# Kernel tuning notes

Hardware: AMD Instinct MI355X
Metric: run time of the kernel (lower is better)

## Reference

```python
import jax, jax.numpy as jnp
import numpy as np

N = 30000
E = 480000
C_IN, H = 16, 4
NEG_SLOPE = 0.2  # PyG GATv2Conv default negative_slope


def gatv2(x, src, dst, Wl, bl, Wr, br, att, bias, heads, outc, concat, n):
    # PyG GATv2Conv (share_weights=False): e_ij = att . leaky_relu(Wl x_j + Wr x_i)
    xl = (x @ Wl + bl).reshape(n, heads, outc)   # source transform
    xr = (x @ Wr + br).reshape(n, heads, outc)   # target transform
    e = jax.nn.leaky_relu(xl[src] + xr[dst], NEG_SLOPE)        # [E,H,C]
    logits = jnp.einsum('ehc,hc->eh', e, att)                  # [E,H]
    m = jax.lax.stop_gradient(jax.ops.segment_max(logits, dst, num_segments=n))
    ex = jnp.exp(logits - m[dst])
    denom = jax.ops.segment_sum(ex, dst, num_segments=n)
    alpha = ex / denom[dst]                                    # scatter-softmax over in-edges
    out = jax.ops.segment_sum(alpha[:, :, None] * xl[src], dst, num_segments=n)  # [N,H,C]
    out = out.reshape(n, heads * outc) if concat else out.mean(axis=1)
    return out + bias


def setup_inputs() -> dict:
    key = jax.random.key(0)
    ks = jax.random.split(key, 16)
    s = 0.05
    inp = {
        'x': jax.random.uniform(ks[0], (N, C_IN), dtype=jnp.float32),
        'edge_index': jax.random.randint(ks[1], (2, E), 0, N, dtype=jnp.int32),
        'lower_bound': jnp.zeros((C_IN,), jnp.float32),
        'upper_bound': jnp.ones((C_IN,), jnp.float32),
        # Layer 1: GATv2Conv(16 -> 32 per head, heads=4, concat=True) => 128
        'W1l': jax.random.normal(ks[2], (C_IN, H * 32), jnp.float32) * s,
        'b1l': jnp.zeros((H * 32,), jnp.float32),
        'W1r': jax.random.normal(ks[3], (C_IN, H * 32), jnp.float32) * s,
        'b1r': jnp.zeros((H * 32,), jnp.float32),
        'att1': jax.random.normal(ks[4], (H, 32), jnp.float32) * s,
        'bias1': jnp.zeros((H * 32,), jnp.float32),
        # Layer 2: GATv2Conv(128 -> 64 per head, heads=4, concat=False) => 64
        'W2l': jax.random.normal(ks[5], (128, H * 64), jnp.float32) * s,
        'b2l': jnp.zeros((H * 64,), jnp.float32),
        'W2r': jax.random.normal(ks[6], (128, H * 64), jnp.float32) * s,
        'b2r': jnp.zeros((H * 64,), jnp.float32),
        'att2': jax.random.normal(ks[7], (H, 64), jnp.float32) * s,
        'bias2': jnp.zeros((64,), jnp.float32),
        # Final linear head 64 -> 5
        'W3': jax.random.normal(ks[8], (64, 5), jnp.float32) * s,
        'b3': jnp.zeros((5,), jnp.float32),
    }
    return inp


def reference(x, edge_index, lower_bound, upper_bound,
              W1l, b1l, W1r, b1r, att1, bias1,
              W2l, b2l, W2r, b2r, att2, bias2,
              W3, b3):
    n = x.shape[0]
    # min-max normalization
    y = (x - lower_bound) / (upper_bound - lower_bound)
    # add self loops (PyG GATv2Conv default add_self_loops=True)
    loops = jnp.tile(jnp.arange(n, dtype=edge_index.dtype)[None, :], (2, 1))
    ei = jnp.concatenate([edge_index, loops], axis=1)
    src, dst = ei[0], ei[1]
    y = gatv2(y, src, dst, W1l, b1l, W1r, b1r, att1, bias1, H, 32, True, n)
    y = jax.nn.relu(y)
    y = gatv2(y, src, dst, W2l, b2l, W2r, b2r, att2, bias2, H, 64, False, n)
    y = jax.nn.relu(y)
    y = y @ W3 + b3
    return jax.nn.sigmoid(y)
```

## Files before the change

kernel.cpp:

```cpp
#include <hip/hip_runtime.h>

#define H 4
#define D1 128
#define D2 256
#define CIN 16
#define SLOPE 0.2f
#define LOG2E 1.4426950408889634f

typedef short short8v __attribute__((ext_vector_type(8)));
typedef float float4v __attribute__((ext_vector_type(4)));
typedef __fp16 half2v __attribute__((ext_vector_type(2)));

__device__ __forceinline__ unsigned short f2bf(float f) {
    unsigned int u = __float_as_uint(f);
    u += 0x7FFFu + ((u >> 16) & 1u);
    return (unsigned short)(u >> 16);
}
__device__ __forceinline__ half2v pkrtz(float a, float b) {
    return __builtin_amdgcn_cvt_pkrtz(a, b);
}
__device__ __forceinline__ half2v h2_from_u32(unsigned u) {
    return __builtin_bit_cast(half2v, u);
}
__device__ __forceinline__ unsigned u32_from_h2(half2v h) {
    return __builtin_bit_cast(unsigned, h);
}
__device__ __forceinline__ float fdot2(half2v a, half2v b, float c) {
#if __has_builtin(__builtin_amdgcn_fdot2)
    return __builtin_amdgcn_fdot2(a, b, c, false);
#else
    return c + (float)a.x * (float)b.x + (float)a.y * (float)b.y;
#endif
}

__device__ __forceinline__ float dpp_sum16(float x) {
    float t;
    t = __int_as_float(__builtin_amdgcn_mov_dpp(__float_as_int(x), 0xB1, 0xF, 0xF, true));
    x += t;
    t = __int_as_float(__builtin_amdgcn_mov_dpp(__float_as_int(x), 0x4E, 0xF, 0xF, true));
    x += t;
    t = __int_as_float(__builtin_amdgcn_mov_dpp(__float_as_int(x), 0x141, 0xF, 0xF, true));
    x += t;
    t = __int_as_float(__builtin_amdgcn_mov_dpp(__float_as_int(x), 0x140, 0xF, 0xF, true));
    x += t;
    return x;
}

__global__ void k_hist(const int* __restrict__ ei, int E, int ET,
                       int* __restrict__ deg) {
    int idx = blockIdx.x * blockDim.x + threadIdx.x;
    if (idx >= ET) return;
    int dst = (idx < E) ? ei[E + idx] : idx - E;
    atomicAdd(&deg[dst], 1);
}

__global__ __launch_bounds__(1024) void k_scan_one(
        const int* __restrict__ deg, int* __restrict__ rp,
        int* __restrict__ cur, int n) {
    __shared__ int wsum[16];
    int t = threadIdx.x;
    int lane = t & 63, w = t >> 6;
    int base = t * 32;
    int vals[32];
    const int4* dp = (const int4*)deg;
#pragma unroll
    for (int q = 0; q < 8; ++q) {
        int4 v = dp[(base >> 2) + q];
        vals[4 * q + 0] = v.x; vals[4 * q + 1] = v.y;
        vals[4 * q + 2] = v.z; vals[4 * q + 3] = v.w;
    }
    int loc[32];
    int s = 0;
#pragma unroll
    for (int k = 0; k < 32; ++k) {
        int idx = base + k;
        int v = (idx < n) ? vals[k] : 0;
        loc[k] = s;
        s += v;
    }
    int inc = s;
#pragma unroll
    for (int off = 1; off < 64; off <<= 1) {
        int u = __shfl_up(inc, off, 64);
        if (lane >= off) inc += u;
    }
    int excl = inc - s;
    if (lane == 63) wsum[w] = inc;
    __syncthreads();
    if (w == 0) {
        int v = (lane < 16) ? wsum[lane] : 0;
        int winc = v;
#pragma unroll
        for (int off = 1; off < 16; off <<= 1) {
            int u = __shfl_up(winc, off, 64);
            if (lane >= off) winc += u;
        }
        if (lane < 16) wsum[lane] = winc - v;
    }
    __syncthreads();
    int offw = wsum[w] + excl;
#pragma unroll
    for (int q = 0; q < 8; ++q) {
        int i0 = base + 4 * q;
        if (i0 + 3 < n) {
            *(int4*)(rp + i0) = make_int4(offw + loc[4 * q + 0], offw + loc[4 * q + 1],
                                          offw + loc[4 * q + 2], offw + loc[4 * q + 3]);
            *(int4*)(cur + i0) = make_int4(0, 0, 0, 0);
        } else {
#pragma unroll
            for (int e = 0; e < 4; ++e) {
                int idx = i0 + e;
                if (idx < n) { rp[idx] = offw + loc[4 * q + e]; cur[idx] = 0; }
            }
        }
    }
}

__global__ void k_fill(const int* __restrict__ ei, int E, int ET,
                       const int* __restrict__ rp, int* __restrict__ cur,
                       int* __restrict__ eord) {
    int idx = blockIdx.x * blockDim.x + threadIdx.x;
    if (idx >= ET) return;
    int src, dst;
    if (idx < E) { src = ei[idx]; dst = ei[E + idx]; }
    else         { src = dst = idx - E; }
    int pos = atomicAdd(&cur[dst], 1);
    eord[rp[dst] + pos] = src;
}

__global__ __launch_bounds__(256) void k_prep(
        const float* __restrict__ x, const float* __restrict__ lb,
        const float* __restrict__ ub,
        const float* __restrict__ Wl, const float* __restrict__ bl,
        const float* __restrict__ Wr, const float* __restrict__ br,
        unsigned short* __restrict__ xl16, unsigned short* __restrict__ xr16,
        const float* __restrict__ W2l, const float* __restrict__ W2r,
        unsigned short* __restrict__ W2t,
        int* __restrict__ deg, int n, int B1) {
    __shared__ float Wls[CIN][D1];
    __shared__ float Wrs[CIN][D1];
    __shared__ float ys[16][CIN];
    int b = blockIdx.x;
    int t = threadIdx.x;
    if (b >= B1) {
        int rb = b - B1;
        if (rb < 256) {
            int idx = rb * 256 + t;
            int k = idx >> 9, c = idx & 511;
            float v = (c < 256) ? W2l[k * 256 + c] : W2r[k * 256 + (c - 256)];
            W2t[(size_t)c * 128 + k] = f2bf(v);
        } else {
            int idx = (rb - 256) * 256 + t;
            if (idx < n) deg[idx] = 0;
        }
        return;
    }
    int i0 = b * 16;
#pragma unroll
    for (int i = 0; i < 8; ++i) {
        int flat = t + 256 * i;
        int k = flat >> 7, c = flat & 127;
        Wls[k][c] = Wl[k * D1 + c];
        Wrs[k][c] = Wr[k * D1 + c];
    }
    {
        int node = t >> 4, k = t & 15;
        int gi = i0 + node;
        float xv = (gi < n) ? x[(size_t)gi * CIN + k] : 0.f;
        ys[node][k] = (xv - lb[k]) / (ub[k] - lb[k]);
    }
    __syncthreads();
    int c = t & 127;
    bool left = t < 128;
    const float (*Ws)[D1] = left ? Wls : Wrs;
    float bias = left ? bl[c] : br[c];
    unsigned short* obuf = left ? xl16 : xr16;
    for (int j = 0; j < 16; ++j) {
        float acc = bias;
#pragma unroll
        for (int k = 0; k < CIN; ++k) acc += ys[j][k] * Ws[k][c];
        int gi = i0 + j;
        float other = __shfl_xor(acc, 1);
        if (gi < n && !(c & 1))
            *(unsigned*)(obuf + (size_t)gi * D1 + c) = u32_from_h2(pkrtz(acc, other));
    }
}

__global__ __launch_bounds__(256) void k_lin2_mfma(
        const unsigned short* __restrict__ h1b,
        const unsigned short* __restrict__ W2t,
        const float* __restrict__ b2l, const float* __restrict__ b2r,
        unsigned short* __restrict__ xl2,
        unsigned short* __restrict__ xr2,
        int n) {
    __shared__ unsigned short At[128 * 128];
    __shared__ unsigned short Bt[128 * 128];
    int t = threadIdx.x;
    int row0 = blockIdx.x * 128;
    int col0 = blockIdx.y * 128;

    {
        int r = t >> 1, hh = (t & 1) * 64;
        bool ok = (row0 + r) < n;
        const unsigned short* gA = h1b + (size_t)(row0 + r) * 128 + hh;
        const unsigned short* gB = W2t + (size_t)(col0 + r) * 128 + hh;
#pragma unroll
        for (int i = 0; i < 8; ++i) {
            uint4 vA = ok ? *(const uint4*)(gA + i * 8) : make_uint4(0, 0, 0, 0);
            uint4 vB = *(const uint4*)(gB + i * 8);
            int col = hh + i * 8;
            int idx = (r * 128 + col) ^ ((r & 15) << 3);
            *(uint4*)&At[idx] = vA;
            *(uint4*)&Bt[idx] = vB;
        }
    }
    __syncthreads();

    int w = t >> 6, l = t & 63;
    int wr = w >> 1, wc = w & 1;
    float4v acc[4][4];
#pragma unroll
    for (int m = 0; m < 4; ++m)
#pragma unroll
        for (int nn = 0; nn < 4; ++nn) acc[m][nn] = (float4v)0.f;

#pragma unroll
    for (int ks = 0; ks < 4; ++ks) {
        int kb = ks * 32 + ((l >> 4) << 3);
        short8v a[4], b[4];
#pragma unroll
        for (int m = 0; m < 4; ++m) {
            int r = wr * 64 + m * 16 + (l & 15);
            a[m] = *(const short8v*)&At[(r * 128 + kb) ^ ((r & 15) << 3)];
        }
#pragma unroll
        for (int nn = 0; nn < 4; ++nn) {
            int c = wc * 64 + nn * 16 + (l & 15);
            b[nn] = *(const short8v*)&Bt[(c * 128 + kb) ^ ((c & 15) << 3)];
        }
#pragma unroll
        for (int m = 0; m < 4; ++m)
#pragma unroll
            for (int nn = 0; nn < 4; ++nn)
                acc[m][nn] = __builtin_amdgcn_mfma_f32_16x16x32_bf16(
                    a[m], b[nn], acc[m][nn], 0, 0, 0);
    }

    unsigned short* ob = (col0 < 256) ? xl2 : xr2;
    const float* bp = (col0 < 256) ? b2l : b2r;
    int cb = (col0 < 256) ? col0 : col0 - 256;
#pragma unroll
    for (int nn = 0; nn < 4; ++nn) {
        int colc = cb + wc * 64 + nn * 16 + (l & 15);
        float bv = bp[colc];
#pragma unroll
        for (int m = 0; m < 4; ++m) {
            int rbase = row0 + wr * 64 + m * 16 + ((l >> 4) << 2);
#pragma unroll
            for (int r = 0; r < 4; ++r) {
                int row = rbase + r;
                float val = acc[m][nn][r] + bv;
                float other = __shfl_xor(val, 1);
                if (!(l & 1) && row < n)
                    *(unsigned*)(ob + (size_t)row * 256 + colc) =
                        u32_from_h2(pkrtz(val, other));
            }
        }
    }
}

__global__ __launch_bounds__(256) void k_agg1(
        const unsigned short* __restrict__ xl16, const unsigned short* __restrict__ xr16,
        const float* __restrict__ att, const float* __restrict__ bias,
        const int* __restrict__ rp, const int* __restrict__ deg,
        const int* __restrict__ eord, unsigned short* __restrict__ h1b, int n) {
    int t = threadIdx.x;
    int node = blockIdx.x * 4 + (t >> 6);
    int l = t & 63;
    int nd = (node < n) ? node : n - 1;
    half2v xr01 = h2_from_u32(((const unsigned*)xr16)[(size_t)nd * 64 + l]);
    float2 av = *(const float2*)(att + 2 * l);
    half2v av01 = pkrtz(av.x * LOG2E, av.y * LOG2E);
    half2v slp = pkrtz(SLOPE, SLOPE);
    int start = __builtin_amdgcn_readfirstlane(rp[nd]);
    int cnt   = (node < n) ? deg[nd] : 0;
    cnt = __builtin_amdgcn_readfirstlane(cnt);
    const unsigned* xlp = (const unsigned*)xl16;
    float d = 0.f;
    half2v a01 = pkrtz(0.f, 0.f);
    int cnt4 = cnt & ~3;
    unsigned r0, r1, r2, r3;
    if (cnt4 > 0) {
        int i0 = eord[start + 0], i1 = eord[start + 1];
        int i2 = eord[start + 2], i3 = eord[start + 3];
        r0 = xlp[(size_t)i0 * 64 + l]; r1 = xlp[(size_t)i1 * 64 + l];
        r2 = xlp[(size_t)i2 * 64 + l]; r3 = xlp[(size_t)i3 * 64 + l];
    }
    for (int j = 0; j < cnt4; j += 4) {
        half2v x0 = h2_from_u32(r0), x1 = h2_from_u32(r1);
        half2v x2 = h2_from_u32(r2), x3 = h2_from_u32(r3);
        int jn = j + 4;
        if (jn < cnt4) {
            int i0 = eord[start + jn + 0], i1 = eord[start + jn + 1];
            int i2 = eord[start + jn + 2], i3 = eord[start + jn + 3];
            r0 = xlp[(size_t)i0 * 64 + l]; r1 = xlp[(size_t)i1 * 64 + l];
            r2 = xlp[(size_t)i2 * 64 + l]; r3 = xlp[(size_t)i3 * 64 + l];
        }
        half2v s0 = x0 + xr01, s1 = x1 + xr01, s2 = x2 + xr01, s3 = x3 + xr01;
        s0 = __builtin_elementwise_max(s0, s0 * slp);
        s1 = __builtin_elementwise_max(s1, s1 * slp);
        s2 = __builtin_elementwise_max(s2, s2 * slp);
        s3 = __builtin_elementwise_max(s3, s3 * slp);
        float lg0 = fdot2(av01, s0, 0.f);
        float lg1 = fdot2(av01, s1, 0.f);
        float lg2 = fdot2(av01, s2, 0.f);
        float lg3 = fdot2(av01, s3, 0.f);
        lg0 = dpp_sum16(lg0); lg1 = dpp_sum16(lg1);
        lg2 = dpp_sum16(lg2); lg3 = dpp_sum16(lg3);
        float e0 = exp2f(lg0), e1 = exp2f(lg1);
        float e2 = exp2f(lg2), e3 = exp2f(lg3);
        d += (e0 + e1) + (e2 + e3);
        a01 += pkrtz(e0, e0) * x0;
        a01 += pkrtz(e1, e1) * x1;
        a01 += pkrtz(e2, e2) * x2;
        a01 += pkrtz(e3, e3) * x3;
    }
    for (int j = cnt4; j < cnt; ++j) {
        int s0i = eord[start + j];
        half2v x0 = h2_from_u32(xlp[(size_t)s0i * 64 + l]);
        half2v s0 = x0 + xr01;
        s0 = __builtin_elementwise_max(s0, s0 * slp);
        float lg0 = fdot2(av01, s0, 0.f);
        lg0 = dpp_sum16(lg0);
        float e0 = exp2f(lg0);
        d += e0;
        a01 += pkrtz(e0, e0) * x0;
    }
    if (node < n) {
        float inv = 1.f / d;
        float o0 = fmaxf((float)a01.x * inv + bias[2 * l + 0], 0.f);
        float o1 = fmaxf((float)a01.y * inv + bias[2 * l + 1], 0.f);
        ((unsigned*)h1b)[(size_t)node * 64 + l] =
            ((unsigned)f2bf(o1) << 16) | f2bf(o0);
    }
}

__global__ __launch_bounds__(256) void k_agg2(
        const unsigned short* __restrict__ xl16, const unsigned short* __restrict__ xr16,
        const float* __restrict__ att, const float* __restrict__ b2,
        const float* __restrict__ W3, const float* __restrict__ b3,
        const int* __restrict__ rp, const int* __restrict__ deg,
        const int* __restrict__ eord, float* __restrict__ out, int n) {
    int t = threadIdx.x;
    int node = blockIdx.x * 4 + (t >> 6);
    int l = t & 63;
    int nd = (node < n) ? node : n - 1;
    uint2 xru = ((const uint2*)xr16)[(size_t)nd * 64 + l];
    half2v xr01 = h2_from_u32(xru.x), xr23 = h2_from_u32(xru.y);
    float4 av = *(const float4*)(att + 4 * l);
    half2v av01 = pkrtz(av.x * LOG2E, av.y * LOG2E);
    half2v av23 = pkrtz(av.z * LOG2E, av.w * LOG2E);
    half2v slp = pkrtz(SLOPE, SLOPE);
    int start = __builtin_amdgcn_readfirstlane(rp[nd]);
    int cnt   = (node < n) ? deg[nd] : 0;
    cnt = __builtin_amdgcn_readfirstlane(cnt);
    const uint2* xlp = (const uint2*)xl16;
    float d = 0.f;
    half2v a01 = pkrtz(0.f, 0.f), a23 = pkrtz(0.f, 0.f);
    int cnt4 = cnt & ~3;
    uint2 r0, r1, r2, r3;
    if (cnt4 > 0) {
        int i0 = eord[start + 0], i1 = eord[start + 1];
        int i2 = eord[start + 2], i3 = eord[start + 3];
        r0 = xlp[(size_t)i0 * 64 + l]; r1 = xlp[(size_t)i1 * 64 + l];
        r2 = xlp[(size_t)i2 * 64 + l]; r3 = xlp[(size_t)i3 * 64 + l];
    }
    for (int j = 0; j < cnt4; j += 4) {
        half2v x00 = h2_from_u32(r0.x), x01p = h2_from_u32(r0.y);
        half2v x10 = h2_from_u32(r1.x), x11p = h2_from_u32(r1.y);
        half2v x20 = h2_from_u32(r2.x), x21p = h2_from_u32(r2.y);
        half2v x30 = h2_from_u32(r3.x), x31p = h2_from_u32(r3.y);
        int jn = j + 4;
        if (jn < cnt4) {
            int i0 = eord[start + jn + 0], i1 = eord[start + jn + 1];
            int i2 = eord[start + jn + 2], i3 = eord[start + jn + 3];
            r0 = xlp[(size_t)i0 * 64 + l]; r1 = xlp[(size_t)i1 * 64 + l];
            r2 = xlp[(size_t)i2 * 64 + l]; r3 = xlp[(size_t)i3 * 64 + l];
        }
        half2v s;
        float lg0, lg1, lg2, lg3;
        s = x00 + xr01; s = __builtin_elementwise_max(s, s * slp);
        lg0 = fdot2(av01, s, 0.f);
        s = x01p + xr23; s = __builtin_elementwise_max(s, s * slp);
        lg0 = fdot2(av23, s, lg0);
        s = x10 + xr01; s = __builtin_elementwise_max(s, s * slp);
        lg1 = fdot2(av01, s, 0.f);
        s = x11p + xr23; s = __builtin_elementwise_max(s, s * slp);
        lg1 = fdot2(av23, s, lg1);
        s = x20 + xr01; s = __builtin_elementwise_max(s, s * slp);
        lg2 = fdot2(av01, s, 0.f);
        s = x21p + xr23; s = __builtin_elementwise_max(s, s * slp);
        lg2 = fdot2(av23, s, lg2);
        s = x30 + xr01; s = __builtin_elementwise_max(s, s * slp);
        lg3 = fdot2(av01, s, 0.f);
        s = x31p + xr23; s = __builtin_elementwise_max(s, s * slp);
        lg3 = fdot2(av23, s, lg3);
        lg0 = dpp_sum16(lg0); lg1 = dpp_sum16(lg1);
        lg2 = dpp_sum16(lg2); lg3 = dpp_sum16(lg3);
        float e0 = exp2f(lg0), e1 = exp2f(lg1);
        float e2 = exp2f(lg2), e3 = exp2f(lg3);
        d += (e0 + e1) + (e2 + e3);
        half2v ep;
        ep = pkrtz(e0, e0); a01 += ep * x00; a23 += ep * x01p;
        ep = pkrtz(e1, e1); a01 += ep * x10; a23 += ep * x11p;
        ep = pkrtz(e2, e2); a01 += ep * x20; a23 += ep * x21p;
        ep = pkrtz(e3, e3); a01 += ep * x30; a23 += ep * x31p;
    }
    for (int j = cnt4; j < cnt; ++j) {
        int s0i = eord[start + j];
        uint2 p0 = xlp[(size_t)s0i * 64 + l];
        half2v x00 = h2_from_u32(p0.x), x01p = h2_from_u32(p0.y);
        half2v s;
        float lg0;
        s = x00 + xr01; s = __builtin_elementwise_max(s, s * slp);
        lg0 = fdot2(av01, s, 0.f);
        s = x01p + xr23; s = __builtin_elementwise_max(s, s * slp);
        lg0 = fdot2(av23, s, lg0);
        lg0 = dpp_sum16(lg0);
        float e0 = exp2f(lg0);
        d += e0;
        half2v ep = pkrtz(e0, e0);
        a01 += ep * x00; a23 += ep * x01p;
    }
    float inv = 1.f / d;
    float v0 = (float)a01.x * inv, v1 = (float)a01.y * inv;
    float v2 = (float)a23.x * inv, v3 = (float)a23.y * inv;
    v0 += __shfl_xor(v0, 16); v1 += __shfl_xor(v1, 16);
    v2 += __shfl_xor(v2, 16); v3 += __shfl_xor(v3, 16);
    v0 += __shfl_xor(v0, 32); v1 += __shfl_xor(v1, 32);
    v2 += __shfl_xor(v2, 32); v3 += __shfl_xor(v3, 32);
    int c0 = 4 * (l & 15);
    v0 = fmaxf(0.25f * v0 + b2[c0 + 0], 0.f);
    v1 = fmaxf(0.25f * v1 + b2[c0 + 1], 0.f);
    v2 = fmaxf(0.25f * v2 + b2[c0 + 2], 0.f);
    v3 = fmaxf(0.25f * v3 + b2[c0 + 3], 0.f);
    float p0, p1, p2, p3, p4;
    {
        const float* w0 = W3 + (c0 + 0) * 5;
        const float* w1 = W3 + (c0 + 1) * 5;
        const float* w2 = W3 + (c0 + 2) * 5;
        const float* w3 = W3 + (c0 + 3) * 5;
        p0 = v0 * w0[0] + v1 * w1[0] + v2 * w2[0] + v3 * w3[0];
        p1 = v0 * w0[1] + v1 * w1[1] + v2 * w2[1] + v3 * w3[1];
        p2 = v0 * w0[2] + v1 * w1[2] + v2 * w2[2] + v3 * w3[2];
        p3 = v0 * w0[3] + v1 * w1[3] + v2 * w2[3] + v3 * w3[3];
        p4 = v0 * w0[4] + v1 * w1[4] + v2 * w2[4] + v3 * w3[4];
    }
    p0 = dpp_sum16(p0); p1 = dpp_sum16(p1); p2 = dpp_sum16(p2);
    p3 = dpp_sum16(p3); p4 = dpp_sum16(p4);
    if (l == 0 && node < n) {
        float* o = out + (size_t)node * 5;
        o[0] = 1.f / (1.f + __expf(-(p0 + b3[0])));
        o[1] = 1.f / (1.f + __expf(-(p1 + b3[1])));
        o[2] = 1.f / (1.f + __expf(-(p2 + b3[2])));
        o[3] = 1.f / (1.f + __expf(-(p3 + b3[3])));
        o[4] = 1.f / (1.f + __expf(-(p4 + b3[4])));
    }
}

extern "C" void kernel_launch(void* const* d_in, const int* in_sizes, int n_in,
                              void* d_out, int out_size, void* d_ws, size_t ws_size,
                              hipStream_t stream) {
    const float* x     = (const float*)d_in[0];
    const int*   ei    = (const int*)d_in[1];
    const float* lb    = (const float*)d_in[2];
    const float* ub    = (const float*)d_in[3];
    const float* W1l   = (const float*)d_in[4];
    const float* b1l   = (const float*)d_in[5];
    const float* W1r   = (const float*)d_in[6];
    const float* b1r   = (const float*)d_in[7];
    const float* att1  = (const float*)d_in[8];
    const float* bias1 = (const float*)d_in[9];
    const float* W2l   = (const float*)d_in[10];
    const float* b2l   = (const float*)d_in[11];
    const float* W2r   = (const float*)d_in[12];
    const float* b2r   = (const float*)d_in[13];
    const float* att2  = (const float*)d_in[14];
    const float* bias2 = (const float*)d_in[15];
    const float* W3    = (const float*)d_in[16];
    const float* b3    = (const float*)d_in[17];

    int n  = in_sizes[0] / CIN;
    int E  = in_sizes[1] / 2;
    int ET = E + n;

    char* ws = (char*)d_ws;
    size_t off = 0;
    auto alloc = [&](size_t nbytes) {
        void* p = ws + off;
        off += (nbytes + 255) & ~(size_t)255;
        return p;
    };
    unsigned short* xl1 = (unsigned short*)alloc((size_t)n * D1 * 2);
    unsigned short* xr1 = (unsigned short*)alloc((size_t)n * D1 * 2);
    unsigned short* h1b = (unsigned short*)alloc((size_t)n * D1 * 2);
    unsigned short* xl2 = (unsigned short*)alloc((size_t)n * D2 * 2);
    unsigned short* xr2 = (unsigned short*)alloc((size_t)n * D2 * 2);
    unsigned short* W2t = (unsigned short*)alloc((size_t)512 * 128 * 2);
    int* deg  = (int*)alloc((size_t)n * 4 + 8192);
    int* cur  = (int*)alloc((size_t)n * 4);
    int* rp   = (int*)alloc((size_t)n * 4);
    int* eord = (int*)alloc((size_t)ET * 4);

    int B1 = (n + 15) / 16;
    int BZ = (n + 255) / 256;
    k_prep<<<B1 + 256 + BZ, 256, 0, stream>>>(
        x, lb, ub, W1l, b1l, W1r, b1r, xl1, xr1, W2l, W2r, W2t, deg, n, B1);

    k_hist<<<(ET + 255) / 256, 256, 0, stream>>>(ei, E, ET, deg);
    k_scan_one<<<1, 1024, 0, stream>>>(deg, rp, cur, n);
    k_fill<<<(ET + 255) / 256, 256, 0, stream>>>(ei, E, ET, rp, cur, eord);

    k_agg1<<<(n + 3) / 4, 256, 0, stream>>>(xl1, xr1, att1, bias1, rp, deg,
                                            eord, h1b, n);

    dim3 g2((n + 127) / 128, 4);
    k_lin2_mfma<<<g2, 256, 0, stream>>>(h1b, W2t, b2l, b2r, xl2, xr2, n);
    k_agg2<<<(n + 3) / 4, 256, 0, stream>>>(xl2, xr2, att2, bias2, W3, b3,
                                            rp, deg, eord, (float*)d_out, n);
}
```

Measured before the change: 171.6 us.

## Store gathered source features in FP8 and process nodes in degree-sorted order

The per-edge gathered source-side features (xl for both layers) are now stored as FP8 (e4m3) instead of FP16, halving the bytes read in the random gather of the aggregation kernels, and are converted back to half on load. In addition, the single-block scan kernel builds a degree-descending node ordering via a shared-memory counting sort, and both aggregation kernels map waves to nodes through this ordering so that wavefronts in a block have similar edge counts. The FP8 storage reduces precision of the attention inputs and messages, which risks accuracy beyond tolerance, and the sort adds serial work to the single-block scan kernel.

After: 170.6 us. No clear change (-0.6%).

```diff
diff --git a/kernel.cpp b/kernel.cpp
--- a/kernel.cpp
+++ b/kernel.cpp
@@ -9,6 +9,7 @@
 
 typedef short short8v __attribute__((ext_vector_type(8)));
 typedef float float4v __attribute__((ext_vector_type(4)));
+typedef float float2v __attribute__((ext_vector_type(2)));
 typedef __fp16 half2v __attribute__((ext_vector_type(2)));
 
 __device__ __forceinline__ unsigned short f2bf(float f) {
@@ -24,6 +25,18 @@
 }
 __device__ __forceinline__ unsigned u32_from_h2(half2v h) {
     return __builtin_bit_cast(unsigned, h);
+}
+__device__ __forceinline__ unsigned short f2fp8x2(float a, float b) {
+    return (unsigned short)__builtin_amdgcn_cvt_pk_fp8_f32(a, b, 0, false);
+}
+template<bool HI>
+__device__ __forceinline__ half2v fp8x2_to_h2(unsigned u) {
+#if __has_builtin(__builtin_amdgcn_cvt_scalef32_pk_f16_fp8)
+    return __builtin_amdgcn_cvt_scalef32_pk_f16_fp8(u, 1.f, HI);
+#else
+    float2v f = __builtin_amdgcn_cvt_pk_f32_fp8(u, HI);
+    return pkrtz(f.x, f.y);
+#endif
 }
 __device__ __forceinline__ float fdot2(half2v a, half2v b, float c) {
 #if __has_builtin(__builtin_amdgcn_fdot2)
@@ -56,10 +69,12 @@
 
 __global__ __launch_bounds__(1024) void k_scan_one(
         const int* __restrict__ deg, int* __restrict__ rp,
-        int* __restrict__ cur, int n) {
+        int* __restrict__ cur, int* __restrict__ ord, int n) {
     __shared__ int wsum[16];
+    __shared__ int dh[256];
     int t = threadIdx.x;
     int lane = t & 63, w = t >> 6;
+    if (t < 256) dh[t] = 0;
     int base = t * 32;
     int vals[32];
     const int4* dp = (const int4*)deg;
@@ -112,6 +127,38 @@
                 int idx = i0 + e;
                 if (idx < n) { rp[idx] = offw + loc[4 * q + e]; cur[idx] = 0; }
             }
+        }
+    }
+#pragma unroll
+    for (int k = 0; k < 32; ++k) {
+        int idx = base + k;
+        if (idx < n) {
+            int bin = 255 - min(vals[k], 255);
+            atomicAdd(&dh[bin], 1);
+        }
+    }
+    __syncthreads();
+    if (t < 64) {
+        int b0 = dh[4 * t], b1 = dh[4 * t + 1], b2 = dh[4 * t + 2], b3 = dh[4 * t + 3];
+        int s4 = b0 + b1 + b2 + b3;
+        int inc2 = s4;
+#pragma unroll
+        for (int off = 1; off < 64; off <<= 1) {
+            int u = __shfl_up(inc2, off, 64);
+            if (lane >= off) inc2 += u;
+        }
+        int ex = inc2 - s4;
+        dh[4 * t] = ex; dh[4 * t + 1] = ex + b0;
+        dh[4 * t + 2] = ex + b0 + b1; dh[4 * t + 3] = ex + b0 + b1 + b2;
+    }
+    __syncthreads();
+#pragma unroll
+    for (int k = 0; k < 32; ++k) {
+        int idx = base + k;
+        if (idx < n) {
+            int bin = 255 - min(vals[k], 255);
+            int pos = atomicAdd(&dh[bin], 1);
+            ord[pos] = idx;
         }
     }
 }
@@ -133,7 +180,7 @@
         const float* __restrict__ ub,
         const float* __restrict__ Wl, const float* __restrict__ bl,
         const float* __restrict__ Wr, const float* __restrict__ br,
-        unsigned short* __restrict__ xl16, unsigned short* __restrict__ xr16,
+        unsigned char* __restrict__ xl8, unsigned short* __restrict__ xr16,
         const float* __restrict__ W2l, const float* __restrict__ W2r,
         unsigned short* __restrict__ W2t,
         int* __restrict__ deg, int n, int B1) {
@@ -174,15 +221,18 @@
     bool left = t < 128;
     const float (*Ws)[D1] = left ? Wls : Wrs;
     float bias = left ? bl[c] : br[c];
-    unsigned short* obuf = left ? xl16 : xr16;
     for (int j = 0; j < 16; ++j) {
         float acc = bias;
 #pragma unroll
         for (int k = 0; k < CIN; ++k) acc += ys[j][k] * Ws[k][c];
         int gi = i0 + j;
         float other = __shfl_xor(acc, 1);
-        if (gi < n && !(c & 1))
-            *(unsigned*)(obuf + (size_t)gi * D1 + c) = u32_from_h2(pkrtz(acc, other));
+        if (gi < n && !(c & 1)) {
+            if (left)
+                *(unsigned short*)(xl8 + (size_t)gi * D1 + c) = f2fp8x2(acc, other);
+            else
+                *(unsigned*)(xr16 + (size_t)gi * D1 + c) = u32_from_h2(pkrtz(acc, other));
+        }
     }
 }
 
@@ -190,7 +240,7 @@
         const unsigned short* __restrict__ h1b,
         const unsigned short* __restrict__ W2t,
         const float* __restrict__ b2l, const float* __restrict__ b2r,
-        unsigned short* __restrict__ xl2,
+        unsigned char* __restrict__ xl2,
         unsigned short* __restrict__ xr2,
         int n) {
     __shared__ unsigned short At[128 * 128];
@@ -246,46 +296,70 @@
                     a[m], b[nn], acc[m][nn], 0, 0, 0);
     }
 
-    unsigned short* ob = (col0 < 256) ? xl2 : xr2;
-    const float* bp = (col0 < 256) ? b2l : b2r;
-    int cb = (col0 < 256) ? col0 : col0 - 256;
-#pragma unroll
-    for (int nn = 0; nn < 4; ++nn) {
-        int colc = cb + wc * 64 + nn * 16 + (l & 15);
-        float bv = bp[colc];
-#pragma unroll
-        for (int m = 0; m < 4; ++m) {
-            int rbase = row0 + wr * 64 + m * 16 + ((l >> 4) << 2);
-#pragma unroll
-            for (int r = 0; r < 4; ++r) {
-                int row = rbase + r;
-                float val = acc[m][nn][r] + bv;
-                float other = __shfl_xor(val, 1);
-                if (!(l & 1) && row < n)
-                    *(unsigned*)(ob + (size_t)row * 256 + colc) =
-                        u32_from_h2(pkrtz(val, other));
+    if (col0 < 256) {
+        const float* bp = b2l;
+        int cb = col0;
+#pragma unroll
+        for (int nn = 0; nn < 4; ++nn) {
+            int colc = cb + wc * 64 + nn * 16 + (l & 15);
+            float bv = bp[colc];
+#pragma unroll
+            for (int m = 0; m < 4; ++m) {
+                int rbase = row0 + wr * 64 + m * 16 + ((l >> 4) << 2);
+#pragma unroll
+                for (int r = 0; r < 4; ++r) {
+                    int row = rbase + r;
+                    float val = acc[m][nn][r] + bv;
+                    float other = __shfl_xor(val, 1);
+                    if (!(l & 1) && row < n)
+                        *(unsigned short*)(xl2 + (size_t)row * 256 + colc) =
+                            f2fp8x2(val, other);
+                }
             }
         }
+    } else {
+        const float* bp = b2r;
+        int cb = col0 - 256;
+#pragma unroll
+        for (int nn = 0; nn < 4; ++nn) {
+            int colc = cb + wc * 64 + nn * 16 + (l & 15);
+            float bv = bp[colc];
+#pragma unroll
+            for (int m = 0; m < 4; ++m) {
+                int rbase = row0 + wr * 64 + m * 16 + ((l >> 4) << 2);
+#pragma unroll
+                for (int r = 0; r < 4; ++r) {
+                    int row = rbase + r;
+                    float val = acc[m][nn][r] + bv;
+                    float other = __shfl_xor(val, 1);
+                    if (!(l & 1) && row < n)
+                        *(unsigned*)(xr2 + (size_t)row * 256 + colc) =
+                            u32_from_h2(pkrtz(val, other));
+                }
+            }
+        }
     }
 }
 
 __global__ __launch_bounds__(256) void k_agg1(
-        const unsigned short* __restrict__ xl16, const unsigned short* __restrict__ xr16,
+        const unsigned char* __restrict__ xl8, const unsigned short* __restrict__ xr16,
         const float* __restrict__ att, const float* __restrict__ bias,
         const int* __restrict__ rp, const int* __restrict__ deg,
-        const int* __restrict__ eord, unsigned short* __restrict__ h1b, int n) {
+        const int* __restrict__ eord, const int* __restrict__ ord,
+        unsigned short* __restrict__ h1b, int n) {
     int t = threadIdx.x;
-    int node = blockIdx.x * 4 + (t >> 6);
+    int node0 = blockIdx.x * 4 + (t >> 6);
     int l = t & 63;
-    int nd = (node < n) ? node : n - 1;
-    half2v xr01 = h2_from_u32(((const unsigned*)xr16)[(size_t)nd * 64 + l]);
+    bool valid = node0 < n;
+    int node = ord[valid ? node0 : n - 1];
+    half2v xr01 = h2_from_u32(((const unsigned*)xr16)[(size_t)node * 64 + l]);
     float2 av = *(const float2*)(att + 2 * l);
     half2v av01 = pkrtz(av.x * LOG2E, av.y * LOG2E);
     half2v slp = pkrtz(SLOPE, SLOPE);
-    int start = __builtin_amdgcn_readfirstlane(rp[nd]);
-    int cnt   = (node < n) ? deg[nd] : 0;
+    int start = __builtin_amdgcn_readfirstlane(rp[node]);
+    int cnt   = valid ? deg[node] : 0;
     cnt = __builtin_amdgcn_readfirstlane(cnt);
-    const unsigned* xlp = (const unsigned*)xl16;
+    const unsigned short* xlp = (const unsigned short*)xl8;
     float d = 0.f;
     half2v a01 = pkrtz(0.f, 0.f);
     int cnt4 = cnt & ~3;
@@ -297,8 +371,8 @@
         r2 = xlp[(size_t)i2 * 64 + l]; r3 = xlp[(size_t)i3 * 64 + l];
     }
     for (int j = 0; j < cnt4; j += 4) {
-        half2v x0 = h2_from_u32(r0), x1 = h2_from_u32(r1);
-        half2v x2 = h2_from_u32(r2), x3 = h2_from_u32(r3);
+        half2v x0 = fp8x2_to_h2<false>(r0), x1 = fp8x2_to_h2<false>(r1);
+        half2v x2 = fp8x2_to_h2<false>(r2), x3 = fp8x2_to_h2<false>(r3);
         int jn = j + 4;
         if (jn < cnt4) {
             int i0 = eord[start + jn + 0], i1 = eord[start + jn + 1];
@@ -327,7 +401,7 @@
     }
     for (int j = cnt4; j < cnt; ++j) {
         int s0i = eord[start + j];
-        half2v x0 = h2_from_u32(xlp[(size_t)s0i * 64 + l]);
+        half2v x0 = fp8x2_to_h2<false>((unsigned)xlp[(size_t)s0i * 64 + l]);
         half2v s0 = x0 + xr01;
         s0 = __builtin_elementwise_max(s0, s0 * slp);
         float lg0 = fdot2(av01, s0, 0.f);
@@ -336,7 +410,7 @@
         d += e0;
         a01 += pkrtz(e0, e0) * x0;
     }
-    if (node < n) {
+    if (valid) {
         float inv = 1.f / d;
         float o0 = fmaxf((float)a01.x * inv + bias[2 * l + 0], 0.f);
         float o1 = fmaxf((float)a01.y * inv + bias[2 * l + 1], 0.f);
@@ -346,29 +420,31 @@
 }
 
 __global__ __launch_bounds__(256) void k_agg2(
-        const unsigned short* __restrict__ xl16, const unsigned short* __restrict__ xr16,
+        const unsigned char* __restrict__ xl8, const unsigned short* __restrict__ xr16,
         const float* __restrict__ att, const float* __restrict__ b2,
         const float* __restrict__ W3, const float* __restrict__ b3,
         const int* __restrict__ rp, const int* __restrict__ deg,
-        const int* __restrict__ eord, float* __restrict__ out, int n) {
+        const int* __restrict__ eord, const int* __restrict__ ord,
+        float* __restrict__ out, int n) {
     int t = threadIdx.x;
-    int node = blockIdx.x * 4 + (t >> 6);
+    int node0 = blockIdx.x * 4 + (t >> 6);
     int l = t & 63;
-    int nd = (node < n) ? node : n - 1;
-    uint2 xru = ((const uint2*)xr16)[(size_t)nd * 64 + l];
+    bool valid = node0 < n;
+    int node = ord[valid ? node0 : n - 1];
+    uint2 xru = ((const uint2*)xr16)[(size_t)node * 64 + l];
     half2v xr01 = h2_from_u32(xru.x), xr23 = h2_from_u32(xru.y);
     float4 av = *(const float4*)(att + 4 * l);
     half2v av01 = pkrtz(av.x * LOG2E, av.y * LOG2E);
     half2v av23 = pkrtz(av.z * LOG2E, av.w * LOG2E);
     half2v slp = pkrtz(SLOPE, SLOPE);
-    int start = __builtin_amdgcn_readfirstlane(rp[nd]);
-    int cnt   = (node < n) ? deg[nd] : 0;
+    int start = __builtin_amdgcn_readfirstlane(rp[node]);
+    int cnt   = valid ? deg[node] : 0;
     cnt = __builtin_amdgcn_readfirstlane(cnt);
-    const uint2* xlp = (const uint2*)xl16;
+    const unsigned* xlp = (const unsigned*)xl8;
     float d = 0.f;
     half2v a01 = pkrtz(0.f, 0.f), a23 = pkrtz(0.f, 0.f);
     int cnt4 = cnt & ~3;
-    uint2 r0, r1, r2, r3;
+    unsigned r0, r1, r2, r3;
     if (cnt4 > 0) {
         int i0 = eord[start + 0], i1 = eord[start + 1];
         int i2 = eord[start + 2], i3 = eord[start + 3];
@@ -376,10 +452,10 @@
         r2 = xlp[(size_t)i2 * 64 + l]; r3 = xlp[(size_t)i3 * 64 + l];
     }
     for (int j = 0; j < cnt4; j += 4) {
-        half2v x00 = h2_from_u32(r0.x), x01p = h2_from_u32(r0.y);
-        half2v x10 = h2_from_u32(r1.x), x11p = h2_from_u32(r1.y);
-        half2v x20 = h2_from_u32(r2.x), x21p = h2_from_u32(r2.y);
-        half2v x30 = h2_from_u32(r3.x), x31p = h2_from_u32(r3.y);
+        half2v x00 = fp8x2_to_h2<false>(r0), x01p = fp8x2_to_h2<true>(r0);
+        half2v x10 = fp8x2_to_h2<false>(r1), x11p = fp8x2_to_h2<true>(r1);
+        half2v x20 = fp8x2_to_h2<false>(r2), x21p = fp8x2_to_h2<true>(r2);
+        half2v x30 = fp8x2_to_h2<false>(r3), x31p = fp8x2_to_h2<true>(r3);
         int jn = j + 4;
         if (jn < cnt4) {
             int i0 = eord[start + jn + 0], i1 = eord[start + jn + 1];
@@ -418,8 +494,8 @@
     }
     for (int j = cnt4; j < cnt; ++j) {
         int s0i = eord[start + j];
-        uint2 p0 = xlp[(size_t)s0i * 64 + l];
-        half2v x00 = h2_from_u32(p0.x), x01p = h2_from_u32(p0.y);
+        unsigned p0 = xlp[(size_t)s0i * 64 + l];
+        half2v x00 = fp8x2_to_h2<false>(p0), x01p = fp8x2_to_h2<true>(p0);
         half2v s;
         float lg0;
         s = x00 + xr01; s = __builtin_elementwise_max(s, s * slp);
@@ -458,7 +534,7 @@
     }
     p0 = dpp_sum16(p0); p1 = dpp_sum16(p1); p2 = dpp_sum16(p2);
     p3 = dpp_sum16(p3); p4 = dpp_sum16(p4);
-    if (l == 0 && node < n) {
+    if (l == 0 && valid) {
         float* o = out + (size_t)node * 5;
         o[0] = 1.f / (1.f + __expf(-(p0 + b3[0])));
         o[1] = 1.f / (1.f + __expf(-(p1 + b3[1])));
@@ -501,15 +577,16 @@
         off += (nbytes + 255) & ~(size_t)255;
         return p;
     };
-    unsigned short* xl1 = (unsigned short*)alloc((size_t)n * D1 * 2);
+    unsigned char*  xl1 = (unsigned char*)alloc((size_t)n * D1);
     unsigned short* xr1 = (unsigned short*)alloc((size_t)n * D1 * 2);
     unsigned short* h1b = (unsigned short*)alloc((size_t)n * D1 * 2);
-    unsigned short* xl2 = (unsigned short*)alloc((size_t)n * D2 * 2);
+    unsigned char*  xl2 = (unsigned char*)alloc((size_t)n * D2);
     unsigned short* xr2 = (unsigned short*)alloc((size_t)n * D2 * 2);
     unsigned short* W2t = (unsigned short*)alloc((size_t)512 * 128 * 2);
     int* deg  = (int*)alloc((size_t)n * 4 + 8192);
     int* cur  = (int*)alloc((size_t)n * 4);
     int* rp   = (int*)alloc((size_t)n * 4);
+    int* ord  = (int*)alloc((size_t)n * 4);
     int* eord = (int*)alloc((size_t)ET * 4);
 
     int B1 = (n + 15) / 16;
@@ -518,14 +595,14 @@
         x, lb, ub, W1l, b1l, W1r, b1r, xl1, xr1, W2l, W2r, W2t, deg, n, B1);
 
     k_hist<<<(ET + 255) / 256, 256, 0, stream>>>(ei, E, ET, deg);
-    k_scan_one<<<1, 1024, 0, stream>>>(deg, rp, cur, n);
+    k_scan_one<<<1, 1024, 0, stream>>>(deg, rp, cur, ord, n);
     k_fill<<<(ET + 255) / 256, 256, 0, stream>>>(ei, E, ET, rp, cur, eord);
 
     k_agg1<<<(n + 3) / 4, 256, 0, stream>>>(xl1, xr1, att1, bias1, rp, deg,
-                                            eord, h1b, n);
+                                            eord, ord, h1b, n);
 
     dim3 g2((n + 127) / 128, 4);
     k_lin2_mfma<<<g2, 256, 0, stream>>>(h1b, W2t, b2l, b2r, xl2, xr2, n);
     k_agg2<<<(n + 3) / 4, 256, 0, stream>>>(xl2, xr2, att2, bias2, W3, b3,
-                                            rp, deg, eord, (float*)d_out, n);
-}
+                                            rp, deg, eord, ord, (float*)d_out, n);
+}
```
